# Kernel optimization log

Hardware: AMD Instinct MI355X
Metric: run time of the kernel (lower is better)

The kernel has to match this reference:

```python
import jax, jax.numpy as jnp
import numpy as np

DIM = 192
HEADS = 8
TIME = 256
HID = int(DIM * 2.66)  # 510
B, H, W = 4, 128, 128


def conv1x1(x, w, b):
    # w: [O, C], pointwise conv as einsum
    return jnp.einsum('bchw,oc->bohw', x, w) + b[None, :, None, None]


def dwconv3(x, w, b):
    # depthwise 3x3, w: [C, 1, 3, 3]
    y = jax.lax.conv_general_dilated(
        x, w, window_strides=(1, 1), padding='SAME',
        feature_group_count=x.shape[1],
        dimension_numbers=('NCHW', 'OIHW', 'NCHW'))
    return y + b[None, :, None, None]


def layernorm(x, w, b, eps=1e-6):
    # channel-wise LN; torch .std() is unbiased (ddof=1)
    C = x.shape[1]
    mean = x.mean(axis=1, keepdims=True)
    var = ((x - mean) ** 2).sum(axis=1, keepdims=True) / (C - 1)
    std = jnp.sqrt(var)
    return w * (x - mean) / (std + eps) + b


def modulate(x, t_emb, tw, tb):
    # time_mlp = Linear(SiLU(t_emb)); scale/shift conditioning
    t = jax.nn.silu(t_emb) @ tw.T + tb  # [B, 2C]
    scale, shift = jnp.split(t, 2, axis=-1)
    return x * (1.0 + scale[:, :, None, None]) + shift[:, :, None, None]


def l2norm(x, eps=1e-12):
    n = jnp.sqrt((x * x).sum(axis=-1, keepdims=True))
    return x / jnp.maximum(n, eps)


def mdta(x, t_emb, temp, qkv_w, qkv_b, dw_w, dw_b, proj_w, proj_b, tw, tb):
    Bn, C, Hh, Ww = x.shape
    x = modulate(x, t_emb, tw, tb)
    qkv = dwconv3(conv1x1(x, qkv_w, qkv_b), dw_w, dw_b)
    q, k, v = jnp.split(qkv, 3, axis=1)
    rs = lambda a: a.reshape(Bn, HEADS, C // HEADS, Hh * Ww)
    q, k, v = l2norm(rs(q)), l2norm(rs(k)), rs(v)
    attn = jnp.einsum('bhcl,bhdl->bhcd', q, k) * temp[None]  # [B,h,c,c]
    attn = jax.nn.softmax(attn, axis=-1)
    out = jnp.einsum('bhcd,bhdl->bhcl', attn, v).reshape(Bn, C, Hh, Ww)
    return conv1x1(out, proj_w, proj_b)


def gdfn(x, t_emb, c1_w, c1_b, dw_w, dw_b, c2_w, c2_b, tw, tb):
    x = modulate(x, t_emb, tw, tb)
    x = dwconv3(conv1x1(x, c1_w, c1_b), dw_w, dw_b)
    x1, x2 = jnp.split(x, 2, axis=1)
    return conv1x1(x1 * x2, c2_w, c2_b)


def setup_inputs() -> dict:
    key = jax.random.key(0)
    ks = jax.random.split(key, 16)
    s = 0.02
    d = {
        'x': jax.random.normal(ks[0], (B, DIM, H, W), jnp.float32),
        't_emb': jax.random.normal(ks[1], (B, TIME), jnp.float32),
        'n1_w': jnp.ones((1, DIM, 1, 1), jnp.float32),
        'n1_b': jnp.zeros((1, DIM, 1, 1), jnp.float32),
        'temp': jnp.ones((HEADS, 1, 1), jnp.float32),
        'a_qkv_w': jax.random.normal(ks[2], (3 * DIM, DIM), jnp.float32) * s,
        'a_qkv_b': jnp.zeros((3 * DIM,), jnp.float32),
        'a_dw_w': jax.random.normal(ks[3], (3 * DIM, 1, 3, 3), jnp.float32) * s,
        'a_dw_b': jnp.zeros((3 * DIM,), jnp.float32),
        'a_proj_w': jax.random.normal(ks[4], (DIM, DIM), jnp.float32) * s,
        'a_proj_b': jnp.zeros((DIM,), jnp.float32),
        'a_t_w': jax.random.normal(ks[5], (2 * DIM, TIME), jnp.float32) * s,
        'a_t_b': jnp.zeros((2 * DIM,), jnp.float32),
        'n2_w': jnp.ones((1, DIM, 1, 1), jnp.float32),
        'n2_b': jnp.zeros((1, DIM, 1, 1), jnp.float32),
        'f_c1_w': jax.random.normal(ks[6], (2 * HID, DIM), jnp.float32) * s,
        'f_c1_b': jnp.zeros((2 * HID,), jnp.float32),
        'f_dw_w': jax.random.normal(ks[7], (2 * HID, 1, 3, 3), jnp.float32) * s,
        'f_dw_b': jnp.zeros((2 * HID,), jnp.float32),
        'f_c2_w': jax.random.normal(ks[8], (DIM, HID), jnp.float32) * s,
        'f_c2_b': jnp.zeros((DIM,), jnp.float32),
        'f_t_w': jax.random.normal(ks[9], (2 * DIM, TIME), jnp.float32) * s,
        'f_t_b': jnp.zeros((2 * DIM,), jnp.float32),
    }
    return d


def reference(x, t_emb, n1_w, n1_b, temp, a_qkv_w, a_qkv_b, a_dw_w, a_dw_b,
              a_proj_w, a_proj_b, a_t_w, a_t_b, n2_w, n2_b,
              f_c1_w, f_c1_b, f_dw_w, f_dw_b, f_c2_w, f_c2_b, f_t_w, f_t_b):
    x = x + mdta(layernorm(x, n1_w, n1_b), t_emb, temp,
                 a_qkv_w, a_qkv_b, a_dw_w, a_dw_b, a_proj_w, a_proj_b, a_t_w, a_t_b)
    x = x + gdfn(layernorm(x, n2_w, n2_b), t_emb,
                 f_c1_w, f_c1_b, f_dw_w, f_dw_b, f_c2_w, f_c2_b, f_t_w, f_t_b)
    return x
```

## Files before the change

kernel.cpp:

```cpp
#include <hip/hip_runtime.h>
#include <math.h>

#define HW 16384

using short8 = __attribute__((ext_vector_type(8))) short;
using f32x4  = __attribute__((ext_vector_type(4))) float;

__device__ __forceinline__ float bf2f(unsigned short u){
  union { unsigned int i; float f; } x; x.i = ((unsigned int)u) << 16; return x.f;
}
__device__ __forceinline__ unsigned short f2bf(float f){
  union { float f; unsigned int i; } x; x.f = f;
  return (unsigned short)((x.i + 0x7FFFu + ((x.i >> 16) & 1u)) >> 16);
}

__global__ void castw_k(const float* __restrict__ in, unsigned short* __restrict__ out, int n){
  int i = blockIdx.x * 256 + threadIdx.x;
  if (i < n) out[i] = f2bf(in[i]);
}
__global__ void castw_pad_k(const float* __restrict__ in, unsigned short* __restrict__ out,
                            int M, int Kin, int Kout){
  int i = blockIdx.x * 256 + threadIdx.x;
  if (i < M * Kout){
    int m = i / Kout, k = i - m * Kout;
    out[i] = (k < Kin) ? f2bf(in[m * Kin + k]) : (unsigned short)0;
  }
}

__global__ void modk(const float* __restrict__ t_emb,
                     const float* __restrict__ aw, const float* __restrict__ ab,
                     const float* __restrict__ fw, const float* __restrict__ fb,
                     float* __restrict__ mod_a, float* __restrict__ mod_f){
  int o = blockIdx.x * 128 + threadIdx.x;
  int b = blockIdx.y;
  const float* w  = blockIdx.z ? fw : aw;
  const float* bi = blockIdx.z ? fb : ab;
  float* outp     = blockIdx.z ? mod_f : mod_a;
  const float* te = t_emb + b * 256;
  float acc = bi[o];
  for (int k = 0; k < 256; ++k){
    float u = te[k];
    float s = u / (1.f + expf(-u));
    acc += s * w[o * 256 + k];
  }
  outp[b * 384 + o] = acc;
}

__global__ __launch_bounds__(256) void lnmod_k(const float* __restrict__ x,
                                               const float* __restrict__ nw, const float* __restrict__ nb,
                                               const float* __restrict__ mod, unsigned short* __restrict__ y){
  int b = blockIdx.y;
  int t = threadIdx.x;
  int pl = t & 63, cg = t >> 6;
  int p = blockIdx.x * 64 + pl;
  const float* xb = x + (size_t)b * 192 * HW + p;
  float s = 0.f, s2 = 0.f;
  #pragma unroll 8
  for (int c = cg * 48; c < cg * 48 + 48; ++c){
    float v = xb[(size_t)c * HW]; s += v; s2 += v * v;
  }
  __shared__ float rs[4][64], rq[4][64];
  rs[cg][pl] = s; rq[cg][pl] = s2;
  __syncthreads();
  float S  = rs[0][pl] + rs[1][pl] + rs[2][pl] + rs[3][pl];
  float S2 = rq[0][pl] + rq[1][pl] + rq[2][pl] + rq[3][pl];
  float mean = S * (1.f / 192.f);
  float var  = (S2 - S * mean) * (1.f / 191.f);
  float rinv = 1.f / (sqrtf(fmaxf(var, 0.f)) + 1e-6f);
  const float* mo = mod + b * 384;
  unsigned short buf[48];
  #pragma unroll 8
  for (int i = 0; i < 48; ++i){
    int c = cg * 48 + i;
    float v = xb[(size_t)c * HW];
    float ln = nw[c] * ((v - mean) * rinv) + nb[c];
    buf[i] = f2bf(ln * (1.f + mo[c]) + mo[192 + c]);
  }
  unsigned short* yb = y + ((size_t)b * HW + p) * 192 + cg * 48;
  #pragma unroll
  for (int i = 0; i < 6; ++i) *(uint4*)(yb + i * 8) = *(const uint4*)(buf + i * 8);
}

__global__ __launch_bounds__(256) void gemm_tn2(const unsigned short* __restrict__ A,
                                                const unsigned short* __restrict__ Bact,
                                                const float* __restrict__ bias,
                                                const float* resid, void* outp,
                                                int M, int K, int nMb, int ofp32){
  const int N = HW;
  __shared__ unsigned short As[2][64 * 32];
  __shared__ unsigned short Bs[2][256 * 32];
  const int G = gridDim.x;
  const int bid = blockIdx.x;
  const int lb = (bid & 7) * (G >> 3) + (bid >> 3);
  const int mb = lb % nMb;
  const int rest = lb / nMb;
  const int n0 = (rest & 63) * 256;
  const int bz = rest >> 6;
  const unsigned short* Bp = Bact + (size_t)bz * N * K;
  const int m0 = mb * 64;
  const int t = threadIdx.x;
  const int w = t >> 6, lane = t & 63;
  const int l16 = lane & 15, quad = lane >> 4;

  const int arow = t >> 2, akc = t & 3;
  int gm = m0 + arow; if (gm > M - 1) gm = M - 1;
  const unsigned short* agp = A + (size_t)gm * K + akc * 8;
  const int aoff = arow * 32 + ((akc ^ (arow & 3)) * 8);
  const int brow = t >> 2, bkc = t & 3;
  const unsigned short* bgp = Bp + (size_t)(n0 + brow) * K + bkc * 8;
  const int bslot = (bkc ^ (brow & 3)) * 8;

  f32x4 acc[4][4];
  #pragma unroll
  for (int i = 0; i < 4; ++i)
    #pragma unroll
    for (int j = 0; j < 4; ++j) acc[i][j] = (f32x4){0.f, 0.f, 0.f, 0.f};

  const int kTiles = K >> 5;
  {
    uint4 va = *(const uint4*)agp;
    *(uint4*)&As[0][aoff] = va;
    #pragma unroll
    for (int i = 0; i < 4; ++i){
      uint4 vb = *(const uint4*)(bgp + (size_t)(64 * i) * K);
      *(uint4*)&Bs[0][(brow + 64 * i) * 32 + bslot] = vb;
    }
  }
  __syncthreads();

  const int fs = (quad ^ (l16 & 3)) * 8;
  for (int kt = 0; kt < kTiles; ++kt){
    const int cur = kt & 1;
    const bool more = (kt + 1 < kTiles);
    uint4 va; uint4 vb[4];
    if (more){
      const int k0 = (kt + 1) * 32;
      va = *(const uint4*)(agp + k0);
      #pragma unroll
      for (int i = 0; i < 4; ++i)
        vb[i] = *(const uint4*)(bgp + (size_t)(64 * i) * K + k0);
    }
    short8 af[4], bfr[4];
    #pragma unroll
    for (int mt = 0; mt < 4; ++mt)
      af[mt] = *(const short8*)&As[cur][(mt * 16 + l16) * 32 + fs];
    #pragma unroll
    for (int nt = 0; nt < 4; ++nt)
      bfr[nt] = *(const short8*)&Bs[cur][(w * 64 + nt * 16 + l16) * 32 + fs];
    #pragma unroll
    for (int nt = 0; nt < 4; ++nt)
      #pragma unroll
      for (int mt = 0; mt < 4; ++mt)
        acc[mt][nt] = __builtin_amdgcn_mfma_f32_16x16x32_bf16(af[mt], bfr[nt], acc[mt][nt], 0, 0, 0);
    if (more){
      *(uint4*)&As[cur ^ 1][aoff] = va;
      #pragma unroll
      for (int i = 0; i < 4; ++i)
        *(uint4*)&Bs[cur ^ 1][(brow + 64 * i) * 32 + bslot] = vb[i];
    }
    __syncthreads();
  }

  #pragma unroll
  for (int mt = 0; mt < 4; ++mt)
    #pragma unroll
    for (int nt = 0; nt < 4; ++nt){
      int n = n0 + w * 64 + nt * 16 + l16;
      #pragma unroll
      for (int r = 0; r < 4; ++r){
        int m = m0 + mt * 16 + quad * 4 + r;
        if (m < M){
          float v = acc[mt][nt][r] + bias[m];
          size_t idx = (size_t)bz * M * N + (size_t)m * N + n;
          if (resid) v += resid[idx];
          if (ofp32) ((float*)outp)[idx] = v;
          else       ((unsigned short*)outp)[idx] = f2bf(v);
        }
      }
    }
}

__global__ __launch_bounds__(256) void dw3_k(const unsigned short* __restrict__ in,
                                             const float* __restrict__ w, const float* __restrict__ bias,
                                             unsigned short* __restrict__ out, int C,
                                             float* __restrict__ qn, float* __restrict__ kn){
  __shared__ unsigned short tile[66 * 128];
  __shared__ float red[4];
  int zc = blockIdx.y;
  int b = zc / C, c = zc - b * C;
  int r0 = blockIdx.x * 64;
  const unsigned short* im = in + ((size_t)(b * C + c)) * HW;
  unsigned short* om = out + ((size_t)(b * C + c)) * HW;
  int t = threadIdx.x;
  #pragma unroll
  for (int i = 0; i < 5; ++i){
    int idx = t + 256 * i;
    if (idx < 1056){
      int lr = idx >> 4, lc = (idx & 15) * 8;
      int gr = r0 - 1 + lr;
      uint4 v = {0u, 0u, 0u, 0u};
      if ((unsigned)gr < 128u) v = *(const uint4*)(im + gr * 128 + lc);
      *(uint4*)&tile[lr * 128 + lc] = v;
    }
  }
  __syncthreads();
  const float* wc = w + c * 9;
  float W[9];
  #pragma unroll
  for (int i = 0; i < 9; ++i) W[i] = wc[i];
  float bs = bias[c];
  float ssq = 0.f;
  #pragma unroll
  for (int i = 0; i < 4; ++i){
    int seg = t + 256 * i;
    int orow = seg >> 4, sc = (seg & 15) * 8;
    float acc[8];
    #pragma unroll
    for (int j = 0; j < 8; ++j) acc[j] = bs;
    #pragma unroll
    for (int rr = 0; rr < 3; ++rr){
      const unsigned short* rp = &tile[(orow + rr) * 128 + sc];
      float v[10];
      v[0] = (sc > 0) ? bf2f(rp[-1]) : 0.f;
      uint4 m = *(const uint4*)rp;
      const unsigned short* mu = (const unsigned short*)&m;
      #pragma unroll
      for (int j = 0; j < 8; ++j) v[j + 1] = bf2f(mu[j]);
      v[9] = (sc < 120) ? bf2f(rp[8]) : 0.f;
      float wa = W[rr * 3], wb = W[rr * 3 + 1], wd = W[rr * 3 + 2];
      #pragma unroll
      for (int j = 0; j < 8; ++j) acc[j] += wa * v[j] + wb * v[j + 1] + wd * v[j + 2];
    }
    unsigned short ob[8];
    #pragma unroll
    for (int j = 0; j < 8; ++j){
      ob[j] = f2bf(acc[j]);
      float q = bf2f(ob[j]);
      ssq += q * q;
    }
    *(uint4*)(om + (r0 + orow) * 128 + sc) = *(uint4*)ob;
  }
  if (c < 384){
    #pragma unroll
    for (int off = 32; off; off >>= 1) ssq += __shfl_down(ssq, off);
    if ((t & 63) == 0) red[t >> 6] = ssq;
    __syncthreads();
    if (t == 0){
      float s = red[0] + red[1] + red[2] + red[3];
      float* dst = (c < 192) ? (qn + b * 192 + c) : (kn + b * 192 + c - 192);
      atomicAdd(dst, s);
    }
  }
}

__global__ __launch_bounds__(256) void dwgate_k(const unsigned short* __restrict__ h,
                                                const float* __restrict__ w, const float* __restrict__ bias,
                                                unsigned short* __restrict__ g){
  __shared__ unsigned short tile[2 * 66 * 128];
  int zc = blockIdx.y;
  int b = zc / 510, j = zc - b * 510;
  int r0 = blockIdx.x * 64;
  const unsigned short* im1 = h + ((size_t)(b * 1020 + j)) * HW;
  const unsigned short* im2 = h + ((size_t)(b * 1020 + 510 + j)) * HW;
  int t = threadIdx.x;
  #pragma unroll
  for (int i = 0; i < 9; ++i){
    int idx = t + 256 * i;
    if (idx < 2112){
      int img = (idx >= 1056) ? 1 : 0;
      int li = idx - img * 1056;
      int lr = li >> 4, lc = (li & 15) * 8;
      int gr = r0 - 1 + lr;
      uint4 v = {0u, 0u, 0u, 0u};
      const unsigned short* im = img ? im2 : im1;
      if ((unsigned)gr < 128u) v = *(const uint4*)(im + gr * 128 + lc);
      *(uint4*)&tile[img * 8448 + lr * 128 + lc] = v;
    }
  }
  __syncthreads();
  float W1[9], W2[9];
  #pragma unroll
  for (int i = 0; i < 9; ++i){ W1[i] = w[j * 9 + i]; W2[i] = w[(510 + j) * 9 + i]; }
  float b1 = bias[j], b2 = bias[510 + j];
  unsigned short* gm = g + ((size_t)(b * 510 + j)) * HW;
  #pragma unroll
  for (int i = 0; i < 4; ++i){
    int seg = t + 256 * i;
    int orow = seg >> 4, sc = (seg & 15) * 8;
    float a1[8], a2[8];
    #pragma unroll
    for (int q = 0; q < 8; ++q){ a1[q] = b1; a2[q] = b2; }
    #pragma unroll
    for (int rr = 0; rr < 3; ++rr){
      #pragma unroll
      for (int img = 0; img < 2; ++img){
        const unsigned short* rp = &tile[img * 8448 + (orow + rr) * 128 + sc];
        float v[10];
        v[0] = (sc > 0) ? bf2f(rp[-1]) : 0.f;
        uint4 m = *(const uint4*)rp;
        const unsigned short* mu = (const unsigned short*)&m;
        #pragma unroll
        for (int q = 0; q < 8; ++q) v[q + 1] = bf2f(mu[q]);
        v[9] = (sc < 120) ? bf2f(rp[8]) : 0.f;
        const float* ww = img ? W2 : W1;
        float* aa = img ? a2 : a1;
        float wa = ww[rr * 3], wb = ww[rr * 3 + 1], wd = ww[rr * 3 + 2];
        #pragma unroll
        for (int q = 0; q < 8; ++q) aa[q] += wa * v[q] + wb * v[q + 1] + wd * v[q + 2];
      }
    }
    unsigned short ob[8];
    #pragma unroll
    for (int q = 0; q < 8; ++q) ob[q] = f2bf(a1[q] * a2[q]);
    *(uint4*)(gm + (r0 + orow) * 128 + sc) = *(uint4*)ob;
  }
}

__global__ __launch_bounds__(256) void tr_k(const unsigned short* __restrict__ in,
                                            unsigned short* __restrict__ out, int C, int Kout){
  __shared__ unsigned short tile[64 * 72];
  int b = blockIdx.z;
  int p0 = blockIdx.x * 64, c0 = blockIdx.y * 64;
  int t = threadIdx.x;
  #pragma unroll
  for (int i = 0; i < 2; ++i){
    int id = t + 256 * i;
    int ch = id >> 3, pc = (id & 7) * 8;
    uint4 v = {0u, 0u, 0u, 0u};
    if (c0 + ch < C) v = *(const uint4*)(in + ((size_t)(b * C + c0 + ch)) * HW + p0 + pc);
    const unsigned short* u = (const unsigned short*)&v;
    #pragma unroll
    for (int j = 0; j < 8; ++j) tile[(pc + j) * 72 + ch] = u[j];
  }
  __syncthreads();
  #pragma unroll
  for (int i = 0; i < 2; ++i){
    int id = t + 256 * i;
    int px = id >> 3, cc = (id & 7) * 8;
    *(uint4*)(out + ((size_t)b * HW + p0 + px) * Kout + c0 + cc) = *(const uint4*)&tile[px * 72 + cc];
  }
}

__global__ __launch_bounds__(64) void qk_k(const unsigned short* __restrict__ qkv_dw, float* __restrict__ part){
  int bh = blockIdx.y; int b = bh >> 3, h = bh & 7;
  int ks = blockIdx.x;
  int lane = threadIdx.x;
  int l16 = lane & 15, quad = lane >> 4;
  const unsigned short* qb = qkv_dw + ((size_t)b * 576 + h * 24) * HW;
  const unsigned short* kb = qkv_dw + ((size_t)b * 576 + 192 + h * 24) * HW;
  f32x4 z = {0.f, 0.f, 0.f, 0.f};
  f32x4 a00 = z, a01 = z, a10 = z, a11 = z;
  for (int st = 0; st < 16; ++st){
    int k0 = ks * 512 + st * 32 + quad * 8;
    short8 qa0 = *(const short8*)(qb + (size_t)l16 * HW + k0);
    short8 qa1 = *(const short8*)(qb + (size_t)(l16 + 16) * HW + k0);
    short8 kb0 = *(const short8*)(kb + (size_t)l16 * HW + k0);
    short8 kb1 = *(const short8*)(kb + (size_t)(l16 + 16) * HW + k0);
    a00 = __builtin_amdgcn_mfma_f32_16x16x32_bf16(qa0, kb0, a00, 0, 0, 0);
    a01 = __builtin_amdgcn_mfma_f32_16x16x32_bf16(qa0, kb1, a01, 0, 0, 0);
    a10 = __builtin_amdgcn_mfma_f32_16x16x32_bf16(qa1, kb0, a10, 0, 0, 0);
    a11 = __builtin_amdgcn_mfma_f32_16x16x32_bf16(qa1, kb1, a11, 0, 0, 0);
  }
  float* pp = part + ((size_t)bh * 32 + ks) * 576;
  #pragma unroll
  for (int r = 0; r < 4; ++r){
    int c0 = quad * 4 + r, c1 = 16 + quad * 4 + r;
    int d0 = l16, d1 = 16 + l16;
    if (c0 < 24 && d0 < 24) pp[c0 * 24 + d0] = a00[r];
    if (c0 < 24 && d1 < 24) pp[c0 * 24 + d1] = a01[r];
    if (c1 < 24 && d0 < 24) pp[c1 * 24 + d0] = a10[r];
    if (c1 < 24 && d1 < 24) pp[c1 * 24 + d1] = a11[r];
  }
}

__global__ void softmax_k(const float* __restrict__ part, const float* __restrict__ qn,
                          const float* __restrict__ kn, const float* __restrict__ temp,
                          float* __restrict__ attn){
  int bh = blockIdx.x; int b = bh >> 3, h = bh & 7;
  int c = threadIdx.x;
  if (c >= 24) return;
  float tmp = temp[h];
  float qv = fmaxf(sqrtf(qn[b * 192 + h * 24 + c]), 1e-12f);
  float row[24];
  #pragma unroll
  for (int d = 0; d < 24; ++d){
    float s = 0.f;
    for (int sp = 0; sp < 32; ++sp) s += part[((size_t)bh * 32 + sp) * 576 + c * 24 + d];
    float kv = fmaxf(sqrtf(kn[b * 192 + h * 24 + d]), 1e-12f);
    row[d] = s * tmp / (qv * kv);
  }
  float mx = row[0];
  #pragma unroll
  for (int d = 1; d < 24; ++d) mx = fmaxf(mx, row[d]);
  float sum = 0.f;
  #pragma unroll
  for (int d = 0; d < 24; ++d){ row[d] = expf(row[d] - mx); sum += row[d]; }
  float inv = 1.f / sum;
  #pragma unroll
  for (int d = 0; d < 24; ++d) attn[(size_t)bh * 576 + c * 24 + d] = row[d] * inv;
}

__global__ __launch_bounds__(256) void av_k(const float* __restrict__ attn,
                                            const unsigned short* __restrict__ qkv_dw,
                                            unsigned short* __restrict__ o){
  int bh = blockIdx.y; int b = bh >> 3, h = bh & 7;
  __shared__ float As[576];
  int t = threadIdx.x;
  for (int i = t; i < 576; i += 256) As[i] = attn[(size_t)bh * 576 + i];
  __syncthreads();
  int p = blockIdx.x * 256 + t;
  const unsigned short* vb = qkv_dw + ((size_t)b * 576 + 384 + h * 24) * HW + p;
  float acc[24];
  #pragma unroll
  for (int c = 0; c < 24; ++c) acc[c] = 0.f;
  #pragma unroll
  for (int d = 0; d < 24; ++d){
    float vv = bf2f(vb[(size_t)d * HW]);
    #pragma unroll
    for (int c = 0; c < 24; ++c) acc[c] += As[c * 24 + d] * vv;
  }
  unsigned short ob[24];
  #pragma unroll
  for (int c = 0; c < 24; ++c) ob[c] = f2bf(acc[c]);
  unsigned short* op = o + ((size_t)b * HW + p) * 192 + h * 24;
  #pragma unroll
  for (int i = 0; i < 3; ++i) *(uint4*)(op + i * 8) = *(const uint4*)(ob + i * 8);
}

extern "C" void kernel_launch(void* const* d_in, const int* in_sizes, int n_in,
                              void* d_out, int out_size, void* d_ws, size_t ws_size,
                              hipStream_t stream){
  (void)in_sizes; (void)n_in; (void)out_size; (void)ws_size;
  const float* x        = (const float*)d_in[0];
  const float* t_emb    = (const float*)d_in[1];
  const float* n1_w     = (const float*)d_in[2];
  const float* n1_b     = (const float*)d_in[3];
  const float* temp     = (const float*)d_in[4];
  const float* a_qkv_w  = (const float*)d_in[5];
  const float* a_qkv_b  = (const float*)d_in[6];
  const float* a_dw_w   = (const float*)d_in[7];
  const float* a_dw_b   = (const float*)d_in[8];
  const float* a_proj_w = (const float*)d_in[9];
  const float* a_proj_b = (const float*)d_in[10];
  const float* a_t_w    = (const float*)d_in[11];
  const float* a_t_b    = (const float*)d_in[12];
  const float* n2_w     = (const float*)d_in[13];
  const float* n2_b     = (const float*)d_in[14];
  const float* f_c1_w   = (const float*)d_in[15];
  const float* f_c1_b   = (const float*)d_in[16];
  const float* f_dw_w   = (const float*)d_in[17];
  const float* f_dw_b   = (const float*)d_in[18];
  const float* f_c2_w   = (const float*)d_in[19];
  const float* f_c2_b   = (const float*)d_in[20];
  const float* f_t_w    = (const float*)d_in[21];
  const float* f_t_b    = (const float*)d_in[22];
  float* out = (float*)d_out;
  char* ws = (char*)d_ws;

  unsigned short* y_buf = (unsigned short*)(ws + 0);
  unsigned short* qkv   = (unsigned short*)(ws + 25165824);
  unsigned short* hbuf  = (unsigned short*)(ws + 25165824);
  unsigned short* gbufT = (unsigned short*)(ws + 25165824);
  unsigned short* qkvd  = (unsigned short*)(ws + 100663296);
  unsigned short* obuf  = (unsigned short*)(ws + 176160768);
  unsigned short* gbuf  = (unsigned short*)(ws + 158859264);
  const size_t S = 225705984;
  float* mod_a = (float*)(ws + S);
  float* mod_f = (float*)(ws + S + 8192);
  float* qn    = (float*)(ws + S + 16384);
  float* kn    = (float*)(ws + S + 20480);
  float* part  = (float*)(ws + S + 24576);
  float* attn  = (float*)(ws + S + 2383872);
  unsigned short* Wq  = (unsigned short*)(ws + S + 2457600);
  unsigned short* Wp  = (unsigned short*)(ws + S + 2678784);
  unsigned short* W1  = (unsigned short*)(ws + S + 2752512);
  unsigned short* W2p = (unsigned short*)(ws + S + 3144192);

  castw_k<<<dim3((110592 + 255) / 256), 256, 0, stream>>>(a_qkv_w, Wq, 110592);
  castw_k<<<dim3((36864 + 255) / 256), 256, 0, stream>>>(a_proj_w, Wp, 36864);
  castw_k<<<dim3((195840 + 255) / 256), 256, 0, stream>>>(f_c1_w, W1, 195840);
  castw_pad_k<<<dim3((98304 + 255) / 256), 256, 0, stream>>>(f_c2_w, W2p, 192, 510, 512);
  modk<<<dim3(3, 4, 2), 128, 0, stream>>>(t_emb, a_t_w, a_t_b, f_t_w, f_t_b, mod_a, mod_f);
  hipMemsetAsync(qn, 0, 2 * 768 * sizeof(float), stream);

  lnmod_k<<<dim3(256, 4), 256, 0, stream>>>(x, n1_w, n1_b, mod_a, y_buf);
  gemm_tn2<<<2304, 256, 0, stream>>>(Wq, y_buf, a_qkv_b, nullptr, qkv, 576, 192, 9, 0);
  dw3_k<<<dim3(2, 2304), 256, 0, stream>>>(qkv, a_dw_w, a_dw_b, qkvd, 576, qn, kn);
  qk_k<<<dim3(32, 32), 64, 0, stream>>>(qkvd, part);
  softmax_k<<<32, 64, 0, stream>>>(part, qn, kn, temp, attn);
  av_k<<<dim3(64, 32), 256, 0, stream>>>(attn, qkvd, obuf);
  gemm_tn2<<<768, 256, 0, stream>>>(Wp, obuf, a_proj_b, x, out, 192, 192, 3, 1);

  lnmod_k<<<dim3(256, 4), 256, 0, stream>>>(out, n2_w, n2_b, mod_f, y_buf);
  gemm_tn2<<<4096, 256, 0, stream>>>(W1, y_buf, f_c1_b, nullptr, hbuf, 1020, 192, 16, 0);
  dwgate_k<<<dim3(2, 2040), 256, 0, stream>>>(hbuf, f_dw_w, f_dw_b, gbuf);
  tr_k<<<dim3(256, 8, 4), 256, 0, stream>>>(gbuf, gbufT, 510, 512);
  gemm_tn2<<<768, 256, 0, stream>>>(W2p, gbufT, f_c2_b, out, out, 192, 512, 3, 1);
}
```

Before: 907.8 us.

## Stage GEMM epilogue through shared memory for coalesced stores and refine LDS swizzle

The GEMM epilogue now writes its accumulators into a reused shared-memory tile, then emits 16-byte coalesced global stores for the bf16 output. For the fp32 path it does the same in two halves, with vectorized bias and residual adds. Previously each lane did scattered 2- or 4-byte stores. The LDS XOR swizzle also changes to mix in higher row bits to reduce bank conflicts on fragment reads. The cost is extra shared-memory traffic and barriers in the epilogue.

```diff
diff --git a/kernel.cpp b/kernel.cpp
--- a/kernel.cpp
+++ b/kernel.cpp
@@ -87,8 +87,7 @@
                                                 const float* resid, void* outp,
                                                 int M, int K, int nMb, int ofp32){
   const int N = HW;
-  __shared__ unsigned short As[2][64 * 32];
-  __shared__ unsigned short Bs[2][256 * 32];
+  __shared__ unsigned short SMEM[20480];
   const int G = gridDim.x;
   const int bid = blockIdx.x;
   const int lb = (bid & 7) * (G >> 3) + (bid >> 3);
@@ -105,10 +104,10 @@
   const int arow = t >> 2, akc = t & 3;
   int gm = m0 + arow; if (gm > M - 1) gm = M - 1;
   const unsigned short* agp = A + (size_t)gm * K + akc * 8;
-  const int aoff = arow * 32 + ((akc ^ (arow & 3)) * 8);
+  const int aoff = arow * 32 + ((akc ^ ((arow ^ (arow >> 2)) & 3)) * 8);
   const int brow = t >> 2, bkc = t & 3;
   const unsigned short* bgp = Bp + (size_t)(n0 + brow) * K + bkc * 8;
-  const int bslot = (bkc ^ (brow & 3)) * 8;
+  const int bslot = (bkc ^ ((brow ^ (brow >> 2)) & 3)) * 8;
 
   f32x4 acc[4][4];
   #pragma unroll
@@ -119,16 +118,16 @@
   const int kTiles = K >> 5;
   {
     uint4 va = *(const uint4*)agp;
-    *(uint4*)&As[0][aoff] = va;
+    *(uint4*)&SMEM[aoff] = va;
     #pragma unroll
     for (int i = 0; i < 4; ++i){
       uint4 vb = *(const uint4*)(bgp + (size_t)(64 * i) * K);
-      *(uint4*)&Bs[0][(brow + 64 * i) * 32 + bslot] = vb;
+      *(uint4*)&SMEM[4096 + (brow + 64 * i) * 32 + bslot] = vb;
     }
   }
   __syncthreads();
 
-  const int fs = (quad ^ (l16 & 3)) * 8;
+  const int fs = (quad ^ ((l16 ^ (l16 >> 2)) & 3)) * 8;
   for (int kt = 0; kt < kTiles; ++kt){
     const int cur = kt & 1;
     const bool more = (kt + 1 < kTiles);
@@ -140,44 +139,87 @@
       for (int i = 0; i < 4; ++i)
         vb[i] = *(const uint4*)(bgp + (size_t)(64 * i) * K + k0);
     }
+    const int abase = cur * 2048;
+    const int bbase = 4096 + cur * 8192;
     short8 af[4], bfr[4];
     #pragma unroll
     for (int mt = 0; mt < 4; ++mt)
-      af[mt] = *(const short8*)&As[cur][(mt * 16 + l16) * 32 + fs];
+      af[mt] = *(const short8*)&SMEM[abase + (mt * 16 + l16) * 32 + fs];
     #pragma unroll
     for (int nt = 0; nt < 4; ++nt)
-      bfr[nt] = *(const short8*)&Bs[cur][(w * 64 + nt * 16 + l16) * 32 + fs];
+      bfr[nt] = *(const short8*)&SMEM[bbase + (w * 64 + nt * 16 + l16) * 32 + fs];
     #pragma unroll
     for (int nt = 0; nt < 4; ++nt)
       #pragma unroll
       for (int mt = 0; mt < 4; ++mt)
         acc[mt][nt] = __builtin_amdgcn_mfma_f32_16x16x32_bf16(af[mt], bfr[nt], acc[mt][nt], 0, 0, 0);
     if (more){
-      *(uint4*)&As[cur ^ 1][aoff] = va;
+      const int nabase = (cur ^ 1) * 2048;
+      const int nbbase = 4096 + (cur ^ 1) * 8192;
+      *(uint4*)&SMEM[nabase + aoff] = va;
       #pragma unroll
       for (int i = 0; i < 4; ++i)
-        *(uint4*)&Bs[cur ^ 1][(brow + 64 * i) * 32 + bslot] = vb[i];
+        *(uint4*)&SMEM[nbbase + (brow + 64 * i) * 32 + bslot] = vb[i];
     }
     __syncthreads();
   }
 
-  #pragma unroll
-  for (int mt = 0; mt < 4; ++mt)
-    #pragma unroll
-    for (int nt = 0; nt < 4; ++nt){
-      int n = n0 + w * 64 + nt * 16 + l16;
-      #pragma unroll
-      for (int r = 0; r < 4; ++r){
-        int m = m0 + mt * 16 + quad * 4 + r;
+  if (!ofp32){
+    unsigned short* T = SMEM;
+    #pragma unroll
+    for (int mt = 0; mt < 4; ++mt)
+      #pragma unroll
+      for (int nt = 0; nt < 4; ++nt)
+        #pragma unroll
+        for (int r = 0; r < 4; ++r){
+          int ml = mt * 16 + quad * 4 + r;
+          int bm = m0 + ml; if (bm > M - 1) bm = M - 1;
+          T[ml * 264 + w * 64 + nt * 16 + l16] = f2bf(acc[mt][nt][r] + bias[bm]);
+        }
+    __syncthreads();
+    unsigned short* ob = (unsigned short*)outp + (size_t)bz * M * N;
+    #pragma unroll
+    for (int i = 0; i < 8; ++i){
+      int c = t + 256 * i;
+      int row = c >> 5, col = (c & 31) * 8;
+      if (m0 + row < M)
+        *(uint4*)(ob + (size_t)(m0 + row) * N + n0 + col) = *(const uint4*)&T[row * 264 + col];
+    }
+  } else {
+    float* T = (float*)&SMEM[0];
+    float* ob = (float*)outp + (size_t)bz * M * N;
+    const float* rb = resid ? resid + (size_t)bz * M * N : nullptr;
+    #pragma unroll
+    for (int half = 0; half < 2; ++half){
+      #pragma unroll
+      for (int mt = 0; mt < 2; ++mt)
+        #pragma unroll
+        for (int nt = 0; nt < 4; ++nt)
+          #pragma unroll
+          for (int r = 0; r < 4; ++r){
+            int ml = mt * 16 + quad * 4 + r;
+            T[ml * 260 + w * 64 + nt * 16 + l16] = acc[half * 2 + mt][nt][r];
+          }
+      __syncthreads();
+      #pragma unroll
+      for (int i = 0; i < 8; ++i){
+        int c = t + 256 * i;
+        int row = c >> 6, col = (c & 63) * 4;
+        int m = m0 + half * 32 + row;
         if (m < M){
-          float v = acc[mt][nt][r] + bias[m];
-          size_t idx = (size_t)bz * M * N + (size_t)m * N + n;
-          if (resid) v += resid[idx];
-          if (ofp32) ((float*)outp)[idx] = v;
-          else       ((unsigned short*)outp)[idx] = f2bf(v);
+          size_t idx = (size_t)m * N + n0 + col;
+          f32x4 v = *(const f32x4*)&T[row * 260 + col];
+          float bv = bias[m];
+          v[0] += bv; v[1] += bv; v[2] += bv; v[3] += bv;
+          if (rb){
+            v[0] += rb[idx]; v[1] += rb[idx + 1]; v[2] += rb[idx + 2]; v[3] += rb[idx + 3];
+          }
+          *(f32x4*)&ob[idx] = v;
         }
       }
-    }
+      __syncthreads();
+    }
+  }
 }
 
 __global__ __launch_bounds__(256) void dw3_k(const unsigned short* __restrict__ in,
@@ -481,7 +523,7 @@
   castw_k<<<dim3((195840 + 255) / 256), 256, 0, stream>>>(f_c1_w, W1, 195840);
   castw_pad_k<<<dim3((98304 + 255) / 256), 256, 0, stream>>>(f_c2_w, W2p, 192, 510, 512);
   modk<<<dim3(3, 4, 2), 128, 0, stream>>>(t_emb, a_t_w, a_t_b, f_t_w, f_t_b, mod_a, mod_f);
-  hipMemsetAsync(qn, 0, 2 * 768 * sizeof(float), stream);
+  (void)hipMemsetAsync(qn, 0, 2 * 768 * sizeof(float), stream);
 
   lnmod_k<<<dim3(256, 4), 256, 0, stream>>>(x, n1_w, n1_b, mod_a, y_buf);
   gemm_tn2<<<2304, 256, 0, stream>>>(Wq, y_buf, a_qkv_b, nullptr, qkv, 576, 192, 9, 0);
```

After: 763.0 us. -15.9%, faster.
